# Performance work log

Measured on AMD Instinct MI355X. Metric: run time of the kernel, lower is better.

Reference implementation:

```python
import jax, jax.numpy as jnp
import numpy as np

NEG_SLOPE = 0.2  # LeakyReLU(0.2) on the final Dense


def setup_inputs() -> dict:
    key = jax.random.key(0)
    k1, k2, k3, k4 = jax.random.split(key, 4)
    B, D = 256, 65536          # batch, input voxel dim
    N, G = 41, 2048            # n_groups, group size (overlapping allowed)
    O, E = 256, 512            # per-group output dim, embed_dim
    x = jax.random.normal(k1, (B, D), dtype=jnp.float32)
    group_idx = jax.random.randint(k2, (N, G), 0, D, dtype=jnp.int32)
    # He-normal-ish init for the per-group Dense weights
    W = jax.random.normal(k3, (N, G, O), dtype=jnp.float32) * np.float32(np.sqrt(2.0 / G))
    b = jnp.zeros((N, O), dtype=jnp.float32)
    W3 = jax.random.normal(k4, (N * O, E), dtype=jnp.float32) * np.float32(np.sqrt(2.0 / (N * O)))
    b3 = jnp.zeros((E,), dtype=jnp.float32)
    return {"x": x, "group_idx": group_idx, "W": W, "b": b, "W3": W3, "b3": b3}


def reference(x, group_idx, W, b, W3, b3):
    B = x.shape[0]
    # per-group gather: (B, N, G)
    g = x[:, group_idx]
    # N parallel Dense layers as one grouped GEMM: (B, N, O)
    h = jnp.einsum('bng,ngo->bno', g, W) + b
    # concat along feature axis -> (B, N*O); dropout is identity at inference
    h = h.reshape(B, -1)
    # final Dense + LeakyReLU(0.2)
    out = h @ W3 + b3
    return jnp.where(out >= 0, out, NEG_SLOPE * out)
```

## Files before the change

kernel.cpp:

```cpp
#include <hip/hip_runtime.h>
#include <hip/hip_bf16.h>

#define NB 256
#define DD 65536
#define NN 41
#define GG 2048
#define OO 256
#define NO 10496
#define EE 512
#define NEG_SLOPE 0.2f

typedef __attribute__((ext_vector_type(8))) short bf16x8;
typedef __attribute__((ext_vector_type(4))) float f32x4;
typedef unsigned int u32;

__device__ __forceinline__ void gl_lds16(const __hip_bfloat16* gsrc, __hip_bfloat16* lds) {
    __builtin_amdgcn_global_load_lds((const __attribute__((address_space(1))) u32*)gsrc,
                                     (__attribute__((address_space(3))) u32*)lds, 16, 0, 0);
}

__global__ __launch_bounds__(256) void transpose_cast_k(const float* __restrict__ src,
                                                        __hip_bfloat16* __restrict__ dst,
                                                        int K, int Oc) {
    __shared__ float tile[32][33];
    size_t slab = (size_t)blockIdx.z * K * Oc;
    int k0 = blockIdx.y * 32, o0 = blockIdx.x * 32;
    int tx = threadIdx.x & 31, ty = threadIdx.x >> 5;
    const float* s = src + slab;
#pragma unroll
    for (int i = 0; i < 4; ++i)
        tile[ty + 8 * i][tx] = s[(size_t)(k0 + ty + 8 * i) * Oc + o0 + tx];
    __syncthreads();
    __hip_bfloat16* d = dst + slab;
    int o = threadIdx.x >> 4;
    int kp = threadIdx.x & 15;
#pragma unroll
    for (int i2 = 0; i2 < 2; ++i2) {
        int oo = o + 16 * i2;
        __hip_bfloat162 p;
        p.x = __float2bfloat16(tile[2 * kp][oo]);
        p.y = __float2bfloat16(tile[2 * kp + 1][oo]);
        *(__hip_bfloat162*)&d[(size_t)(o0 + oo) * K + k0 + 2 * kp] = p;
    }
}

__global__ __launch_bounds__(512) void gather_full_k(const float* __restrict__ x,
                                                     const int* __restrict__ idx,
                                                     __hip_bfloat16* __restrict__ g) {
    extern __shared__ __hip_bfloat16 xr[];
    int b = blockIdx.x;
    int t = threadIdx.x;
    const float4* xv = (const float4*)(x + (size_t)b * DD);
#pragma unroll
    for (int i = 0; i < 32; ++i) {
        float4 v = xv[t + 512 * i];
        short4 p;
        p.x = (short)__bfloat16_as_ushort(__float2bfloat16(v.x));
        p.y = (short)__bfloat16_as_ushort(__float2bfloat16(v.y));
        p.z = (short)__bfloat16_as_ushort(__float2bfloat16(v.z));
        p.w = (short)__bfloat16_as_ushort(__float2bfloat16(v.w));
        *(short4*)&xr[(t + 512 * i) * 4] = p;
    }
    __syncthreads();
    const int4* idx4 = (const int4*)idx;
#pragma unroll 1
    for (int it = 0; it < 41; ++it) {
        int u = t + 512 * it;
        int n = u >> 9;
        int k = (u & 511) * 4;
        int4 ii = idx4[u];
        ushort4 o;
        o.x = __bfloat16_as_ushort(xr[ii.x]);
        o.y = __bfloat16_as_ushort(xr[ii.y]);
        o.z = __bfloat16_as_ushort(xr[ii.z]);
        o.w = __bfloat16_as_ushort(xr[ii.w]);
        *(ushort4*)&g[((size_t)n * NB + b) * GG + k] = o;
    }
}

__global__ __launch_bounds__(512) void gather_half_k(const float* __restrict__ x,
                                                     const int* __restrict__ idx,
                                                     __hip_bfloat16* __restrict__ g) {
    __shared__ __align__(16) __hip_bfloat16 xr[32768];
    int b = blockIdx.x >> 1;
    int h = blockIdx.x & 1;
    int t = threadIdx.x;
    const float4* xv = (const float4*)(x + (size_t)b * DD + h * 32768);
#pragma unroll
    for (int i = 0; i < 16; ++i) {
        float4 v = xv[t + 512 * i];
        short4 p;
        p.x = (short)__bfloat16_as_ushort(__float2bfloat16(v.x));
        p.y = (short)__bfloat16_as_ushort(__float2bfloat16(v.y));
        p.z = (short)__bfloat16_as_ushort(__float2bfloat16(v.z));
        p.w = (short)__bfloat16_as_ushort(__float2bfloat16(v.w));
        *(short4*)&xr[(t + 512 * i) * 4] = p;
    }
    __syncthreads();
    const int4* idx4 = (const int4*)idx;
    for (int u = t; u < NN * GG / 4; u += 512) {
        int4 ii = idx4[u];
        int n = u >> 9;
        int k = (u & 511) * 4;
        __hip_bfloat16* dst = &g[((size_t)n * NB + b) * GG + k];
        if ((ii.x >> 15) == h) dst[0] = xr[ii.x & 32767];
        if ((ii.y >> 15) == h) dst[1] = xr[ii.y & 32767];
        if ((ii.z >> 15) == h) dst[2] = xr[ii.z & 32767];
        if ((ii.w >> 15) == h) dst[3] = xr[ii.w & 32767];
    }
}

__global__ __launch_bounds__(256) void gemm1_k(const __hip_bfloat16* __restrict__ g,
                                               const __hip_bfloat16* __restrict__ Wt,
                                               const float* __restrict__ bias,
                                               __hip_bfloat16* __restrict__ h) {
    int bid = blockIdx.x;
    int n = bid >> 2;
    int m0 = ((bid >> 1) & 1) * 128;
    int o0 = (bid & 1) * 128;
    const __hip_bfloat16* srcA = g + ((size_t)n * NB + m0) * GG;
    const __hip_bfloat16* srcB = Wt + ((size_t)n * OO + o0) * GG;
    __shared__ __align__(16) __hip_bfloat16 lA[128 * 32];
    __shared__ __align__(16) __hip_bfloat16 lB[128 * 32];
    int t = threadIdx.x;
    int lane = t & 63, w = t >> 6;
    int mw = (w >> 1) * 64, nw = (w & 1) * 64;
    int lrow = lane & 15, quad = lane >> 4;
    int r0 = t >> 2, q0 = (t & 3) * 8;
    f32x4 acc[4][4] = {};

    for (int k0 = 0; k0 < GG; k0 += 32) {
        __syncthreads();
        gl_lds16(srcA + (size_t)r0 * GG + k0 + q0, lA + t * 8);
        gl_lds16(srcA + (size_t)(r0 + 64) * GG + k0 + q0, lA + (t + 256) * 8);
        gl_lds16(srcB + (size_t)r0 * GG + k0 + q0, lB + t * 8);
        gl_lds16(srcB + (size_t)(r0 + 64) * GG + k0 + q0, lB + (t + 256) * 8);
        __syncthreads();
        bf16x8 af[4];
#pragma unroll
        for (int fm = 0; fm < 4; ++fm)
            af[fm] = *(const bf16x8*)&lA[(mw + fm * 16 + lrow) * 32 + quad * 8];
#pragma unroll
        for (int fn = 0; fn < 4; ++fn) {
            bf16x8 bfr = *(const bf16x8*)&lB[(nw + fn * 16 + lrow) * 32 + quad * 8];
#pragma unroll
            for (int fm = 0; fm < 4; ++fm)
                acc[fm][fn] = __builtin_amdgcn_mfma_f32_16x16x32_bf16(af[fm], bfr, acc[fm][fn], 0, 0, 0);
        }
    }
#pragma unroll
    for (int fm = 0; fm < 4; ++fm) {
#pragma unroll
        for (int fn = 0; fn < 4; ++fn) {
            int col = o0 + nw + fn * 16 + lrow;
            float bv = bias[n * OO + col];
#pragma unroll
            for (int r = 0; r < 4; ++r) {
                int row = m0 + mw + fm * 16 + quad * 4 + r;
                h[(size_t)row * NO + n * OO + col] = __float2bfloat16(acc[fm][fn][r] + bv);
            }
        }
    }
}

__global__ __launch_bounds__(256) void gemm2_k(const __hip_bfloat16* __restrict__ h,
                                               const __hip_bfloat16* __restrict__ W3t,
                                               float* __restrict__ part) {
    int bid = blockIdx.x;
    int s = bid >> 3;
    int m0 = ((bid >> 2) & 1) * 128;
    int e0 = (bid & 3) * 128;
    const __hip_bfloat16* srcA = h + (size_t)m0 * NO;
    const __hip_bfloat16* srcB = W3t + (size_t)e0 * NO;
    __shared__ __align__(16) __hip_bfloat16 lA[128 * 32];
    __shared__ __align__(16) __hip_bfloat16 lB[128 * 32];
    int t = threadIdx.x;
    int lane = t & 63, w = t >> 6;
    int mw = (w >> 1) * 64, nw = (w & 1) * 64;
    int lrow = lane & 15, quad = lane >> 4;
    int r0 = t >> 2, q0 = (t & 3) * 8;
    f32x4 acc[4][4] = {};

    for (int k0 = s * 256; k0 < s * 256 + 256; k0 += 32) {
        __syncthreads();
        gl_lds16(srcA + (size_t)r0 * NO + k0 + q0, lA + t * 8);
        gl_lds16(srcA + (size_t)(r0 + 64) * NO + k0 + q0, lA + (t + 256) * 8);
        gl_lds16(srcB + (size_t)r0 * NO + k0 + q0, lB + t * 8);
        gl_lds16(srcB + (size_t)(r0 + 64) * NO + k0 + q0, lB + (t + 256) * 8);
        __syncthreads();
        bf16x8 af[4];
#pragma unroll
        for (int fm = 0; fm < 4; ++fm)
            af[fm] = *(const bf16x8*)&lA[(mw + fm * 16 + lrow) * 32 + quad * 8];
#pragma unroll
        for (int fn = 0; fn < 4; ++fn) {
            bf16x8 bfr = *(const bf16x8*)&lB[(nw + fn * 16 + lrow) * 32 + quad * 8];
#pragma unroll
            for (int fm = 0; fm < 4; ++fm)
                acc[fm][fn] = __builtin_amdgcn_mfma_f32_16x16x32_bf16(af[fm], bfr, acc[fm][fn], 0, 0, 0);
        }
    }
#pragma unroll
    for (int fm = 0; fm < 4; ++fm) {
#pragma unroll
        for (int fn = 0; fn < 4; ++fn) {
            int e = e0 + nw + fn * 16 + lrow;
#pragma unroll
            for (int r = 0; r < 4; ++r) {
                int row = m0 + mw + fm * 16 + quad * 4 + r;
                part[((size_t)s * NB + row) * EE + e] = acc[fm][fn][r];
            }
        }
    }
}

__global__ __launch_bounds__(256) void reduce_k(const float* __restrict__ part,
                                                const float* __restrict__ b3,
                                                float* __restrict__ out) {
    int j = blockIdx.x * 256 + threadIdx.x;
    float4 a = make_float4(0.f, 0.f, 0.f, 0.f);
    for (int s = 0; s < NN; ++s) {
        float4 v = ((const float4*)part)[(size_t)s * (NB * EE / 4) + j];
        a.x += v.x; a.y += v.y; a.z += v.z; a.w += v.w;
    }
    float4 bv = ((const float4*)b3)[j & 127];
    a.x += bv.x; a.y += bv.y; a.z += bv.z; a.w += bv.w;
    a.x = a.x >= 0.f ? a.x : NEG_SLOPE * a.x;
    a.y = a.y >= 0.f ? a.y : NEG_SLOPE * a.y;
    a.z = a.z >= 0.f ? a.z : NEG_SLOPE * a.z;
    a.w = a.w >= 0.f ? a.w : NEG_SLOPE * a.w;
    ((float4*)out)[j] = a;
}

extern "C" void kernel_launch(void* const* d_in, const int* in_sizes, int n_in,
                              void* d_out, int out_size, void* d_ws, size_t ws_size,
                              hipStream_t stream) {
    const float* x = (const float*)d_in[0];
    const int* idx = (const int*)d_in[1];
    const float* W = (const float*)d_in[2];
    const float* bias = (const float*)d_in[3];
    const float* W3 = (const float*)d_in[4];
    const float* b3 = (const float*)d_in[5];
    float* out = (float*)d_out;

    char* ws = (char*)d_ws;
    const size_t g_off = 0;
    const size_t g_sz = (size_t)NN * NB * GG * 2;
    const size_t wt_off = g_off + g_sz;
    const size_t wt_sz = (size_t)NN * GG * OO * 2;
    const size_t w3t_off = wt_off + wt_sz;
    const size_t w3t_sz = (size_t)NO * EE * 2;
    const size_t h_off = w3t_off + w3t_sz;
    const size_t h_sz = (size_t)NB * NO * 2;
    const size_t p_off = h_off + h_sz;

    __hip_bfloat16* g = (__hip_bfloat16*)(ws + g_off);
    __hip_bfloat16* Wt = (__hip_bfloat16*)(ws + wt_off);
    __hip_bfloat16* W3t = (__hip_bfloat16*)(ws + w3t_off);
    __hip_bfloat16* h = (__hip_bfloat16*)(ws + h_off);
    float* part = (float*)(ws + p_off);

    transpose_cast_k<<<dim3(OO / 32, GG / 32, NN), 256, 0, stream>>>(W, Wt, GG, OO);
    transpose_cast_k<<<dim3(EE / 32, NO / 32, 1), 256, 0, stream>>>(W3, W3t, NO, EE);
    hipError_t aerr = hipFuncSetAttribute(reinterpret_cast<const void*>(gather_full_k),
                                          hipFuncAttributeMaxDynamicSharedMemorySize, 131072);
    if (aerr == hipSuccess) {
        gather_full_k<<<dim3(NB), 512, 131072, stream>>>(x, idx, g);
    } else {
        gather_half_k<<<dim3(512), 512, 0, stream>>>(x, idx, g);
    }
    gemm1_k<<<dim3(164), 256, 0, stream>>>(g, Wt, bias, h);
    gemm2_k<<<dim3(328), 256, 0, stream>>>(h, W3t, part);
    reduce_k<<<dim3(128), 256, 0, stream>>>(part, b3, out);
}
```

Before: 308.5 us.

## Split-K the grouped GEMM, double-buffer LDS tiles, and widen GEMM blocks

The first grouped GEMM is split into two K halves, giving 328 blocks instead of 164 so more CUs are busy. The halves write fp32 partials, and a new combine kernel adds them with the bias and casts to bf16. Both GEMMs now use 512-thread blocks with double-buffered LDS: the next K tile is fetched while the current one is multiplied, with one barrier per step. The cost is an extra round trip of about 21 MB of fp32 partials and one more kernel launch. The gather loop indexing is also simplified.

```diff
diff --git a/kernel.cpp b/kernel.cpp
--- a/kernel.cpp
+++ b/kernel.cpp
@@ -64,17 +64,14 @@
     __syncthreads();
     const int4* idx4 = (const int4*)idx;
 #pragma unroll 1
-    for (int it = 0; it < 41; ++it) {
-        int u = t + 512 * it;
-        int n = u >> 9;
-        int k = (u & 511) * 4;
-        int4 ii = idx4[u];
+    for (int n = 0; n < NN; ++n) {
+        int4 ii = idx4[n * 512 + t];
         ushort4 o;
         o.x = __bfloat16_as_ushort(xr[ii.x]);
         o.y = __bfloat16_as_ushort(xr[ii.y]);
         o.z = __bfloat16_as_ushort(xr[ii.z]);
         o.w = __bfloat16_as_ushort(xr[ii.w]);
-        *(ushort4*)&g[((size_t)n * NB + b) * GG + k] = o;
+        *(ushort4*)&g[((size_t)n * NB + b) * GG + t * 4] = o;
     }
 }
 
@@ -110,101 +107,134 @@
     }
 }
 
-__global__ __launch_bounds__(256) void gemm1_k(const __hip_bfloat16* __restrict__ g,
+__global__ __launch_bounds__(512) void gemm1_k(const __hip_bfloat16* __restrict__ g,
                                                const __hip_bfloat16* __restrict__ Wt,
-                                               const float* __restrict__ bias,
-                                               __hip_bfloat16* __restrict__ h) {
+                                               float* __restrict__ part1) {
     int bid = blockIdx.x;
-    int n = bid >> 2;
+    int n = bid >> 3;
+    int s = bid & 1;
     int m0 = ((bid >> 1) & 1) * 128;
-    int o0 = (bid & 1) * 128;
-    const __hip_bfloat16* srcA = g + ((size_t)n * NB + m0) * GG;
-    const __hip_bfloat16* srcB = Wt + ((size_t)n * OO + o0) * GG;
-    __shared__ __align__(16) __hip_bfloat16 lA[128 * 32];
-    __shared__ __align__(16) __hip_bfloat16 lB[128 * 32];
+    int o0 = ((bid >> 2) & 1) * 128;
+    const __hip_bfloat16* srcA = g + ((size_t)n * NB + m0) * GG + s * 1024;
+    const __hip_bfloat16* srcB = Wt + ((size_t)n * OO + o0) * GG + s * 1024;
+    __shared__ __align__(16) __hip_bfloat16 lA[2][128 * 32];
+    __shared__ __align__(16) __hip_bfloat16 lB[2][128 * 32];
     int t = threadIdx.x;
     int lane = t & 63, w = t >> 6;
-    int mw = (w >> 1) * 64, nw = (w & 1) * 64;
+    int mw = (w >> 2) * 64;
+    int ow = (w & 3) * 32;
     int lrow = lane & 15, quad = lane >> 4;
     int r0 = t >> 2, q0 = (t & 3) * 8;
-    f32x4 acc[4][4] = {};
-
-    for (int k0 = 0; k0 < GG; k0 += 32) {
-        __syncthreads();
-        gl_lds16(srcA + (size_t)r0 * GG + k0 + q0, lA + t * 8);
-        gl_lds16(srcA + (size_t)(r0 + 64) * GG + k0 + q0, lA + (t + 256) * 8);
-        gl_lds16(srcB + (size_t)r0 * GG + k0 + q0, lB + t * 8);
-        gl_lds16(srcB + (size_t)(r0 + 64) * GG + k0 + q0, lB + (t + 256) * 8);
-        __syncthreads();
+    size_t offA = (size_t)r0 * GG + q0;
+    size_t offB = (size_t)r0 * GG + q0;
+    f32x4 acc[4][2] = {};
+
+    gl_lds16(srcA + offA, &lA[0][t * 8]);
+    gl_lds16(srcB + offB, &lB[0][t * 8]);
+    __syncthreads();
+#pragma unroll 1
+    for (int it = 0; it < 32; ++it) {
+        int cur = it & 1;
+        if (it + 1 < 32) {
+            int k1 = (it + 1) * 32;
+            gl_lds16(srcA + offA + k1, &lA[1 - cur][t * 8]);
+            gl_lds16(srcB + offB + k1, &lB[1 - cur][t * 8]);
+        }
         bf16x8 af[4];
 #pragma unroll
         for (int fm = 0; fm < 4; ++fm)
-            af[fm] = *(const bf16x8*)&lA[(mw + fm * 16 + lrow) * 32 + quad * 8];
-#pragma unroll
-        for (int fn = 0; fn < 4; ++fn) {
-            bf16x8 bfr = *(const bf16x8*)&lB[(nw + fn * 16 + lrow) * 32 + quad * 8];
+            af[fm] = *(const bf16x8*)&lA[cur][(mw + fm * 16 + lrow) * 32 + quad * 8];
+#pragma unroll
+        for (int fn = 0; fn < 2; ++fn) {
+            bf16x8 bfr = *(const bf16x8*)&lB[cur][(ow + fn * 16 + lrow) * 32 + quad * 8];
 #pragma unroll
             for (int fm = 0; fm < 4; ++fm)
                 acc[fm][fn] = __builtin_amdgcn_mfma_f32_16x16x32_bf16(af[fm], bfr, acc[fm][fn], 0, 0, 0);
         }
+        __syncthreads();
     }
 #pragma unroll
     for (int fm = 0; fm < 4; ++fm) {
 #pragma unroll
-        for (int fn = 0; fn < 4; ++fn) {
-            int col = o0 + nw + fn * 16 + lrow;
-            float bv = bias[n * OO + col];
+        for (int fn = 0; fn < 2; ++fn) {
+            int col = o0 + ow + fn * 16 + lrow;
 #pragma unroll
             for (int r = 0; r < 4; ++r) {
                 int row = m0 + mw + fm * 16 + quad * 4 + r;
-                h[(size_t)row * NO + n * OO + col] = __float2bfloat16(acc[fm][fn][r] + bv);
+                part1[((size_t)s * NB + row) * NO + n * OO + col] = acc[fm][fn][r];
             }
         }
     }
 }
 
-__global__ __launch_bounds__(256) void gemm2_k(const __hip_bfloat16* __restrict__ h,
+__global__ __launch_bounds__(256) void combine1_k(const float* __restrict__ part1,
+                                                  const float* __restrict__ bias,
+                                                  __hip_bfloat16* __restrict__ h) {
+    int j4 = blockIdx.x * 256 + threadIdx.x;
+    const float4* p0 = (const float4*)part1;
+    const float4* p1 = p0 + (size_t)NB * NO / 4;
+    int jj = j4 % (NO / 4);
+    float4 a = p0[j4], c = p1[j4];
+    float4 bv = ((const float4*)bias)[jj];
+    a.x += c.x + bv.x; a.y += c.y + bv.y; a.z += c.z + bv.z; a.w += c.w + bv.w;
+    ushort4 o;
+    o.x = __bfloat16_as_ushort(__float2bfloat16(a.x));
+    o.y = __bfloat16_as_ushort(__float2bfloat16(a.y));
+    o.z = __bfloat16_as_ushort(__float2bfloat16(a.z));
+    o.w = __bfloat16_as_ushort(__float2bfloat16(a.w));
+    *(ushort4*)&h[(size_t)j4 * 4] = o;
+}
+
+__global__ __launch_bounds__(512) void gemm2_k(const __hip_bfloat16* __restrict__ h,
                                                const __hip_bfloat16* __restrict__ W3t,
                                                float* __restrict__ part) {
     int bid = blockIdx.x;
     int s = bid >> 3;
     int m0 = ((bid >> 2) & 1) * 128;
     int e0 = (bid & 3) * 128;
-    const __hip_bfloat16* srcA = h + (size_t)m0 * NO;
-    const __hip_bfloat16* srcB = W3t + (size_t)e0 * NO;
-    __shared__ __align__(16) __hip_bfloat16 lA[128 * 32];
-    __shared__ __align__(16) __hip_bfloat16 lB[128 * 32];
+    const __hip_bfloat16* srcA = h + (size_t)m0 * NO + s * 256;
+    const __hip_bfloat16* srcB = W3t + (size_t)e0 * NO + s * 256;
+    __shared__ __align__(16) __hip_bfloat16 lA[2][128 * 32];
+    __shared__ __align__(16) __hip_bfloat16 lB[2][128 * 32];
     int t = threadIdx.x;
     int lane = t & 63, w = t >> 6;
-    int mw = (w >> 1) * 64, nw = (w & 1) * 64;
+    int mw = (w >> 2) * 64;
+    int ew = (w & 3) * 32;
     int lrow = lane & 15, quad = lane >> 4;
     int r0 = t >> 2, q0 = (t & 3) * 8;
-    f32x4 acc[4][4] = {};
-
-    for (int k0 = s * 256; k0 < s * 256 + 256; k0 += 32) {
-        __syncthreads();
-        gl_lds16(srcA + (size_t)r0 * NO + k0 + q0, lA + t * 8);
-        gl_lds16(srcA + (size_t)(r0 + 64) * NO + k0 + q0, lA + (t + 256) * 8);
-        gl_lds16(srcB + (size_t)r0 * NO + k0 + q0, lB + t * 8);
-        gl_lds16(srcB + (size_t)(r0 + 64) * NO + k0 + q0, lB + (t + 256) * 8);
-        __syncthreads();
+    size_t offA = (size_t)r0 * NO + q0;
+    size_t offB = (size_t)r0 * NO + q0;
+    f32x4 acc[4][2] = {};
+
+    gl_lds16(srcA + offA, &lA[0][t * 8]);
+    gl_lds16(srcB + offB, &lB[0][t * 8]);
+    __syncthreads();
+#pragma unroll 1
+    for (int it = 0; it < 8; ++it) {
+        int cur = it & 1;
+        if (it + 1 < 8) {
+            int k1 = (it + 1) * 32;
+            gl_lds16(srcA + offA + k1, &lA[1 - cur][t * 8]);
+            gl_lds16(srcB + offB + k1, &lB[1 - cur][t * 8]);
+        }
         bf16x8 af[4];
 #pragma unroll
         for (int fm = 0; fm < 4; ++fm)
-            af[fm] = *(const bf16x8*)&lA[(mw + fm * 16 + lrow) * 32 + quad * 8];
-#pragma unroll
-        for (int fn = 0; fn < 4; ++fn) {
-            bf16x8 bfr = *(const bf16x8*)&lB[(nw + fn * 16 + lrow) * 32 + quad * 8];
+            af[fm] = *(const bf16x8*)&lA[cur][(mw + fm * 16 + lrow) * 32 + quad * 8];
+#pragma unroll
+        for (int fn = 0; fn < 2; ++fn) {
+            bf16x8 bfr = *(const bf16x8*)&lB[cur][(ew + fn * 16 + lrow) * 32 + quad * 8];
 #pragma unroll
             for (int fm = 0; fm < 4; ++fm)
                 acc[fm][fn] = __builtin_amdgcn_mfma_f32_16x16x32_bf16(af[fm], bfr, acc[fm][fn], 0, 0, 0);
         }
+        __syncthreads();
     }
 #pragma unroll
     for (int fm = 0; fm < 4; ++fm) {
 #pragma unroll
-        for (int fn = 0; fn < 4; ++fn) {
-            int e = e0 + nw + fn * 16 + lrow;
+        for (int fn = 0; fn < 2; ++fn) {
+            int e = e0 + ew + fn * 16 + lrow;
 #pragma unroll
             for (int r = 0; r < 4; ++r) {
                 int row = m0 + mw + fm * 16 + quad * 4 + r;
@@ -258,6 +288,7 @@
     __hip_bfloat16* Wt = (__hip_bfloat16*)(ws + wt_off);
     __hip_bfloat16* W3t = (__hip_bfloat16*)(ws + w3t_off);
     __hip_bfloat16* h = (__hip_bfloat16*)(ws + h_off);
+    float* part1 = (float*)(ws + p_off);
     float* part = (float*)(ws + p_off);
 
     transpose_cast_k<<<dim3(OO / 32, GG / 32, NN), 256, 0, stream>>>(W, Wt, GG, OO);
@@ -269,7 +300,8 @@
     } else {
         gather_half_k<<<dim3(512), 512, 0, stream>>>(x, idx, g);
     }
-    gemm1_k<<<dim3(164), 256, 0, stream>>>(g, Wt, bias, h);
-    gemm2_k<<<dim3(328), 256, 0, stream>>>(h, W3t, part);
+    gemm1_k<<<dim3(328), 512, 0, stream>>>(g, Wt, part1);
+    combine1_k<<<dim3(NB * NO / 4 / 256), 256, 0, stream>>>(part1, bias, h);
+    gemm2_k<<<dim3(328), 512, 0, stream>>>(h, W3t, part);
     reduce_k<<<dim3(128), 256, 0, stream>>>(part, b3, out);
 }
```

Measured after the change: 276.7 us. 10.3% less time.
